# Optimization experiments

Hardware: AMD Instinct MI355X
Metric: run time of the kernel (lower is better)

The kernel has to match this reference:

```python
import jax, jax.numpy as jnp
import numpy as np

HEADS = 8
DIM_HEAD = 64
INNER = HEADS * DIM_HEAD  # 512
DIM = 256
MSA_H = 128  # number of MSA rows
MSA_W = 256  # sequence length


def setup_inputs() -> dict:
    key = jax.random.key(0)
    ks = jax.random.split(key, 8)
    n = MSA_H * MSA_W
    w_std = 0.02
    return {
        "x": jax.random.normal(ks[0], (1, n, DIM), dtype=jnp.float32),
        "wq_w": jax.random.normal(ks[1], (DIM, INNER), dtype=jnp.float32) * w_std,
        "wkv_w": jax.random.normal(ks[2], (DIM, 2 * INNER), dtype=jnp.float32) * w_std,
        "wout_w": jax.random.normal(ks[3], (INNER, DIM), dtype=jnp.float32) * w_std,
        "wout_b": jnp.zeros((DIM,), dtype=jnp.float32),
        "hq_w": jax.random.normal(ks[4], (DIM, INNER), dtype=jnp.float32) * w_std,
        "hkv_w": jax.random.normal(ks[5], (DIM, 2 * INNER), dtype=jnp.float32) * w_std,
        "hout_w": jax.random.normal(ks[6], (INNER, DIM), dtype=jnp.float32) * w_std,
        "hout_b": jnp.zeros((DIM,), dtype=jnp.float32),
        "msa_h": MSA_H,
        "msa_w": MSA_W,
    }


def reference(x, wq_w, wkv_w, wout_w, wout_b, hq_w, hkv_w, hout_w, hout_b, msa_h, msa_w):
    b, n, d = x.shape
    h, w = msa_h, msa_w
    scale = DIM_HEAD ** -0.5
    x4 = x.reshape(b, h, w, d)  # (b, rows, cols, dim)

    # ---- width attention: attend across MSA rows (h), independent per column (w) ----
    xw = jnp.swapaxes(x4, 1, 2)  # (b, w, h, d)
    q = (xw @ wq_w).reshape(b, w, h, HEADS, DIM_HEAD)
    kv = (xw @ wkv_w).reshape(b, w, h, 2, HEADS, DIM_HEAD)
    k, v = kv[..., 0, :, :], kv[..., 1, :, :]
    dots = jnp.einsum('bwiHd,bwjHd->bwHij', q, k) * scale  # (b, w, H, h, h)
    attn = jax.nn.softmax(dots, axis=-1)
    o = jnp.einsum('bwHij,bwjHd->bwiHd', attn, v).reshape(b, w, h, INNER)
    w_out = o @ wout_w + wout_b  # (b, w, h, d)
    w_out = jnp.swapaxes(w_out, 1, 2)  # (b, h, w, d)

    # ---- height attention: attend across columns (w), rows tied (tie_attn_dim = h) ----
    q = (x4 @ hq_w).reshape(b, h, w, HEADS, DIM_HEAD)
    kv = (x4 @ hkv_w).reshape(b, h, w, 2, HEADS, DIM_HEAD)
    k, v = kv[..., 0, :, :], kv[..., 1, :, :]
    tie_scale = scale * (h ** -0.5)
    # scores summed over tied row dim r: 'b r h i d, b r h j d -> b h i j'
    dots = jnp.einsum('briHd,brjHd->bHij', q, k) * tie_scale  # (b, H, w, w)
    attn = jax.nn.softmax(dots, axis=-1)
    o = jnp.einsum('bHij,brjHd->briHd', attn, v).reshape(b, h, w, INNER)
    h_out = o @ hout_w + hout_b  # (b, h, w, d)

    out = w_out + h_out
    return out.reshape(b, h * w, d)
```

## Files before the change

kernel.cpp:

```cpp
#include <hip/hip_runtime.h>

typedef short s16x8 __attribute__((ext_vector_type(8)));
typedef float f32x4 __attribute__((ext_vector_type(4)));

#define MFMA16(a, b, c) __builtin_amdgcn_mfma_f32_16x16x32_bf16((a), (b), (c), 0, 0, 0)

__device__ __forceinline__ unsigned short f2b(float f) {
  union { float f; unsigned int u; } v; v.f = f;
  unsigned int u = v.u;
  unsigned int r = (u + 0x7fffu + ((u >> 16) & 1u)) >> 16;
  return (unsigned short)r;
}
__device__ __forceinline__ float b2f(unsigned short b) {
  union { unsigned int u; float f; } v; v.u = ((unsigned int)b) << 16;
  return v.f;
}

__device__ __forceinline__ void gld_lds16(const void* g, void* l) {
  __builtin_amdgcn_global_load_lds(
      (const __attribute__((address_space(1))) unsigned int*)g,
      (__attribute__((address_space(3))) unsigned int*)l, 16, 0, 0);
}

__global__ __launch_bounds__(256) void cvt_x(const float* __restrict__ x,
                                             unsigned short* __restrict__ xb) {
  size_t i = ((size_t)blockIdx.x * 256 + threadIdx.x) * 4;
  float4 v = *(const float4*)(x + i);
  ushort4 o;
  o.x = f2b(v.x); o.y = f2b(v.y); o.z = f2b(v.z); o.w = f2b(v.w);
  *(ushort4*)(xb + i) = o;
}

__global__ __launch_bounds__(256) void build_wt(const float* __restrict__ wq,
                                                const float* __restrict__ wkv,
                                                const float* __restrict__ hq,
                                                const float* __restrict__ hkv,
                                                unsigned short* __restrict__ WT) {
  const int n = blockIdx.x, k = threadIdx.x;
  float v;
  if (n < 512)       v = wq [(size_t)k * 512  + n];
  else if (n < 1536) v = wkv[(size_t)k * 1024 + (n - 512)];
  else if (n < 2048) v = hq [(size_t)k * 512  + (n - 1536)];
  else               v = hkv[(size_t)k * 1024 + (n - 2048)];
  WT[(size_t)n * 256 + k] = f2b(v);
}

__global__ __launch_bounds__(256) void build_w2t(const float* __restrict__ wout,
                                                 const float* __restrict__ hout,
                                                 unsigned short* __restrict__ W2T) {
  const int n = blockIdx.x;
  for (int k = threadIdx.x; k < 1024; k += 256) {
    const float v = (k < 512) ? wout[(size_t)k * 256 + n] : hout[(size_t)(k - 512) * 256 + n];
    W2T[(size_t)n * 1024 + k] = f2b(v);
  }
}

__global__ __launch_bounds__(256) void gemm_qkv(const unsigned short* __restrict__ X,
                                                const unsigned short* __restrict__ WT,
                                                unsigned short* __restrict__ C,
                                                int branch) {
  __shared__ unsigned short As[128 * 32];
  __shared__ unsigned short Bs[128 * 32];
  const int tid = threadIdx.x, wave = tid >> 6, lane = tid & 63;
  const int q = lane >> 4, l = lane & 15;
  const int m0 = blockIdx.x * 128;
  const int n0 = blockIdx.y * 128;
  const int mt = (wave >> 1) * 64;
  const int nt = (wave & 1) * 64;
  const char* Xb = (const char*)X;
  const char* Wb = (const char*)WT;
  const int srow = wave * 32 + (lane >> 2);
  const int sboff = (lane & 3) * 16;
  char* AsB = (char*)As;
  char* BsB = (char*)Bs;
  f32x4 acc[4][4] = {};
#pragma unroll
  for (int ks = 0; ks < 8; ++ks) {
    const int kb = ks * 64;
    gld_lds16(Xb + (size_t)(m0 + srow) * 512 + kb + sboff, AsB + wave * 2048);
    gld_lds16(Xb + (size_t)(m0 + srow + 16) * 512 + kb + sboff, AsB + wave * 2048 + 1024);
    gld_lds16(Wb + (size_t)(n0 + srow) * 512 + kb + sboff, BsB + wave * 2048);
    gld_lds16(Wb + (size_t)(n0 + srow + 16) * 512 + kb + sboff, BsB + wave * 2048 + 1024);
    __syncthreads();
    s16x8 a[4], b[4];
#pragma unroll
    for (int i = 0; i < 4; ++i) a[i] = *(const s16x8*)(&As[(mt + i * 16 + l) * 32 + q * 8]);
#pragma unroll
    for (int j = 0; j < 4; ++j) b[j] = *(const s16x8*)(&Bs[(nt + j * 16 + l) * 32 + q * 8]);
#pragma unroll
    for (int i = 0; i < 4; ++i)
#pragma unroll
      for (int j = 0; j < 4; ++j) acc[i][j] = MFMA16(b[j], a[i], acc[i][j]);
    __syncthreads();
  }
#pragma unroll
  for (int i = 0; i < 4; ++i) {
    const int m = m0 + mt + i * 16 + l;
    const int mrow = (branch == 0) ? ((m & 255) * 8) : ((m >> 8) * 8);
    const int mcol = (branch == 0) ? (m >> 8) : (m & 255);
    const int mdim = (branch == 0) ? 128 : 256;
#pragma unroll
    for (int j = 0; j < 4; ++j) {
      const int n = n0 + nt + j * 16 + q * 4;
      const int part = n >> 9, H = (n & 511) >> 6, d = n & 63;
      ushort4 o;
      o.x = f2b(acc[i][j][0]); o.y = f2b(acc[i][j][1]);
      o.z = f2b(acc[i][j][2]); o.w = f2b(acc[i][j][3]);
      unsigned short* base = C + (size_t)part * 16777216;
      const size_t idx = ((size_t)(mrow + H) * mdim + mcol) * 64 + d;
      *(ushort4*)(base + idx) = o;
    }
  }
}

__global__ __launch_bounds__(256) void col_attn(const unsigned short* __restrict__ C,
                                                unsigned short* __restrict__ O) {
  __shared__ unsigned short Sp[128 * 136];
  __shared__ unsigned short Vt[64 * 136];
  const int w = blockIdx.x, H = blockIdx.y;
  const int tid = threadIdx.x, wave = tid >> 6, lane = tid & 63;
  const int q = lane >> 4, l = lane & 15;
  const size_t slab = (size_t)(w * 8 + H) * 8192;
  const unsigned short* Qs = C + slab;
  const unsigned short* Ks = C + 16777216 + slab;
  const unsigned short* Vs = C + 33554432 + slab;
  for (int u = tid; u < 1024; u += 256) {
    const int j = u >> 3, db = u & 7;
    s16x8 v = *(const s16x8*)(Vs + j * 64 + db * 8);
#pragma unroll
    for (int t = 0; t < 8; ++t) Vt[(db * 8 + t) * 136 + j] = v[t];
  }
  const int m0 = wave * 32;
  f32x4 acc[2][8] = {};
#pragma unroll
  for (int ks = 0; ks < 2; ++ks) {
    const int kk = ks * 32 + q * 8;
    s16x8 a[2], b[8];
#pragma unroll
    for (int i = 0; i < 2; ++i) a[i] = *(const s16x8*)(Qs + (m0 + i * 16 + l) * 64 + kk);
#pragma unroll
    for (int j = 0; j < 8; ++j) b[j] = *(const s16x8*)(Ks + (j * 16 + l) * 64 + kk);
#pragma unroll
    for (int i = 0; i < 2; ++i)
#pragma unroll
      for (int j = 0; j < 8; ++j) acc[i][j] = MFMA16(a[i], b[j], acc[i][j]);
  }
#pragma unroll
  for (int i = 0; i < 2; ++i)
#pragma unroll
    for (int r = 0; r < 4; ++r) {
      float v[8];
#pragma unroll
      for (int j = 0; j < 8; ++j) v[j] = acc[i][j][r] * 0.125f;
      float mx = fmaxf(fmaxf(fmaxf(v[0], v[1]), fmaxf(v[2], v[3])),
                       fmaxf(fmaxf(v[4], v[5]), fmaxf(v[6], v[7])));
      mx = fmaxf(mx, __shfl_xor(mx, 1));
      mx = fmaxf(mx, __shfl_xor(mx, 2));
      mx = fmaxf(mx, __shfl_xor(mx, 4));
      mx = fmaxf(mx, __shfl_xor(mx, 8));
      float s = 0.f;
#pragma unroll
      for (int j = 0; j < 8; ++j) { v[j] = __expf(v[j] - mx); s += v[j]; }
      s += __shfl_xor(s, 1);
      s += __shfl_xor(s, 2);
      s += __shfl_xor(s, 4);
      s += __shfl_xor(s, 8);
      const float inv = 1.0f / s;
      const int row = m0 + i * 16 + q * 4 + r;
#pragma unroll
      for (int j = 0; j < 8; ++j) Sp[row * 136 + j * 16 + l] = f2b(v[j] * inv);
    }
  __syncthreads();
  f32x4 o[2][4] = {};
#pragma unroll
  for (int ks = 0; ks < 4; ++ks) {
    const int kk = ks * 32 + q * 8;
    s16x8 a[2], b[4];
#pragma unroll
    for (int i = 0; i < 2; ++i) a[i] = *(const s16x8*)(&Sp[(m0 + i * 16 + l) * 136 + kk]);
#pragma unroll
    for (int j = 0; j < 4; ++j) b[j] = *(const s16x8*)(&Vt[(j * 16 + l) * 136 + kk]);
#pragma unroll
    for (int i = 0; i < 2; ++i)
#pragma unroll
      for (int j = 0; j < 4; ++j) o[i][j] = MFMA16(a[i], b[j], o[i][j]);
  }
#pragma unroll
  for (int i = 0; i < 2; ++i)
#pragma unroll
    for (int j = 0; j < 4; ++j)
#pragma unroll
      for (int r = 0; r < 4; ++r) {
        const int row = m0 + i * 16 + q * 4 + r;
        const int d = j * 16 + l;
        O[(size_t)(row * 256 + w) * 1024 + H * 64 + d] = f2b(o[i][j][r]);
      }
}

__global__ __launch_bounds__(256) void row_dots(const unsigned short* __restrict__ C,
                                                float* __restrict__ dp) {
  const int H = blockIdx.z;
  const int r0 = blockIdx.y * 16;
  const int ti = blockIdx.x & 1, tj = blockIdx.x >> 1;
  const int tid = threadIdx.x, wave = tid >> 6, lane = tid & 63;
  const int q = lane >> 4, l = lane & 15;
  const int m0 = ti * 128 + (wave >> 1) * 64;
  const int n0 = tj * 128 + (wave & 1) * 64;
  const unsigned short* Qh = C;
  const unsigned short* Kh = C + 16777216;
  f32x4 acc[4][4] = {};
  for (int ks = 0; ks < 32; ++ks) {
    const int k = ks * 32 + q * 8;
    const int rr = r0 + (k >> 6), d = k & 63;
    const size_t slab = (size_t)(rr * 8 + H) * 16384;
    s16x8 a[4], b[4];
#pragma unroll
    for (int i = 0; i < 4; ++i) a[i] = *(const s16x8*)(Qh + slab + (m0 + i * 16 + l) * 64 + d);
#pragma unroll
    for (int j = 0; j < 4; ++j) b[j] = *(const s16x8*)(Kh + slab + (n0 + j * 16 + l) * 64 + d);
#pragma unroll
    for (int i = 0; i < 4; ++i)
#pragma unroll
      for (int j = 0; j < 4; ++j) acc[i][j] = MFMA16(a[i], b[j], acc[i][j]);
  }
  float* outp = dp + ((size_t)blockIdx.y * 8 + H) * 65536;
#pragma unroll
  for (int i = 0; i < 4; ++i)
#pragma unroll
    for (int j = 0; j < 4; ++j)
#pragma unroll
      for (int r = 0; r < 4; ++r)
        outp[(size_t)(m0 + i * 16 + q * 4 + r) * 256 + n0 + j * 16 + l] = acc[i][j][r];
}

__global__ __launch_bounds__(256) void row_softmax(const float* __restrict__ dp,
                                                   unsigned short* __restrict__ attn) {
  const int row = blockIdx.x;
  const int H = row >> 8, i = row & 255;
  const int t = threadIdx.x, wave = t >> 6, lane = t & 63;
  __shared__ float red[8];
  float v = 0.f;
#pragma unroll
  for (int c = 0; c < 8; ++c) v += dp[((size_t)c * 8 + H) * 65536 + (size_t)i * 256 + t];
  v *= 1.1048543456e-2f;
  float m = v;
  for (int o = 32; o > 0; o >>= 1) m = fmaxf(m, __shfl_xor(m, o, 64));
  if (lane == 0) red[wave] = m;
  __syncthreads();
  const float M = fmaxf(fmaxf(red[0], red[1]), fmaxf(red[2], red[3]));
  const float e = __expf(v - M);
  float s = e;
  for (int o = 32; o > 0; o >>= 1) s += __shfl_xor(s, o, 64);
  if (lane == 0) red[4 + wave] = s;
  __syncthreads();
  const float S = red[4] + red[5] + red[6] + red[7];
  attn[(size_t)row * 256 + t] = f2b(e / S);
}

__global__ __launch_bounds__(256) void row_pv(const unsigned short* __restrict__ C,
                                              const unsigned short* __restrict__ attn,
                                              unsigned short* __restrict__ O) {
  __shared__ unsigned short Vt[64 * 264];
  const int r = blockIdx.x, H = blockIdx.y;
  const int tid = threadIdx.x, wave = tid >> 6, lane = tid & 63;
  const int q = lane >> 4, l = lane & 15;
  const unsigned short* Vs = C + 33554432 + (size_t)(r * 8 + H) * 16384;
  for (int u = tid; u < 2048; u += 256) {
    const int j = u >> 3, db = u & 7;
    s16x8 v = *(const s16x8*)(Vs + j * 64 + db * 8);
#pragma unroll
    for (int t = 0; t < 8; ++t) Vt[(db * 8 + t) * 264 + j] = v[t];
  }
  __syncthreads();
  const unsigned short* A = attn + (size_t)H * 65536;
  const int m0 = wave * 64;
  f32x4 acc[4][4] = {};
#pragma unroll
  for (int ks = 0; ks < 8; ++ks) {
    const int kk = ks * 32 + q * 8;
    s16x8 a[4], b[4];
#pragma unroll
    for (int i = 0; i < 4; ++i) a[i] = *(const s16x8*)(A + (size_t)(m0 + i * 16 + l) * 256 + kk);
#pragma unroll
    for (int j = 0; j < 4; ++j) b[j] = *(const s16x8*)(&Vt[(j * 16 + l) * 264 + kk]);
#pragma unroll
    for (int i = 0; i < 4; ++i)
#pragma unroll
      for (int j = 0; j < 4; ++j) acc[i][j] = MFMA16(a[i], b[j], acc[i][j]);
  }
#pragma unroll
  for (int i = 0; i < 4; ++i)
#pragma unroll
    for (int j = 0; j < 4; ++j)
#pragma unroll
      for (int rr = 0; rr < 4; ++rr) {
        const int iw = m0 + i * 16 + q * 4 + rr;
        const int d = j * 16 + l;
        O[(size_t)(r * 256 + iw) * 1024 + 512 + H * 64 + d] = f2b(acc[i][j][rr]);
      }
}

__global__ __launch_bounds__(256) void out_proj(const unsigned short* __restrict__ O,
                                                const unsigned short* __restrict__ W2T,
                                                const float* __restrict__ bw,
                                                const float* __restrict__ bh,
                                                float* __restrict__ out) {
  __shared__ unsigned short As[128 * 32];
  __shared__ unsigned short Bs[128 * 32];
  const int tid = threadIdx.x, wave = tid >> 6, lane = tid & 63;
  const int q = lane >> 4, l = lane & 15;
  const int m0 = blockIdx.x * 128;
  const int n0 = blockIdx.y * 128;
  const int mt = (wave >> 1) * 64;
  const int nt = (wave & 1) * 64;
  const char* Ob = (const char*)O;
  const char* Wb = (const char*)W2T;
  const int srow = wave * 32 + (lane >> 2);
  const int sboff = (lane & 3) * 16;
  char* AsB = (char*)As;
  char* BsB = (char*)Bs;
  f32x4 acc[4][4] = {};
  for (int ks = 0; ks < 32; ++ks) {
    const int kb = ks * 64;
    gld_lds16(Ob + (size_t)(m0 + srow) * 2048 + kb + sboff, AsB + wave * 2048);
    gld_lds16(Ob + (size_t)(m0 + srow + 16) * 2048 + kb + sboff, AsB + wave * 2048 + 1024);
    gld_lds16(Wb + (size_t)(n0 + srow) * 2048 + kb + sboff, BsB + wave * 2048);
    gld_lds16(Wb + (size_t)(n0 + srow + 16) * 2048 + kb + sboff, BsB + wave * 2048 + 1024);
    __syncthreads();
    s16x8 a[4], b[4];
#pragma unroll
    for (int i = 0; i < 4; ++i) a[i] = *(const s16x8*)(&As[(mt + i * 16 + l) * 32 + q * 8]);
#pragma unroll
    for (int j = 0; j < 4; ++j) b[j] = *(const s16x8*)(&Bs[(nt + j * 16 + l) * 32 + q * 8]);
#pragma unroll
    for (int i = 0; i < 4; ++i)
#pragma unroll
      for (int j = 0; j < 4; ++j) acc[i][j] = MFMA16(b[j], a[i], acc[i][j]);
    __syncthreads();
  }
#pragma unroll
  for (int i = 0; i < 4; ++i) {
    const int m = m0 + mt + i * 16 + l;
#pragma unroll
    for (int j = 0; j < 4; ++j) {
      const int col = n0 + nt + j * 16 + q * 4;
      const float4 bwv = *(const float4*)(bw + col);
      const float4 bhv = *(const float4*)(bh + col);
      float4 ov;
      ov.x = acc[i][j][0] + bwv.x + bhv.x;
      ov.y = acc[i][j][1] + bwv.y + bhv.y;
      ov.z = acc[i][j][2] + bwv.z + bhv.z;
      ov.w = acc[i][j][3] + bwv.w + bhv.w;
      *(float4*)(out + (size_t)m * 256 + col) = ov;
    }
  }
}

extern "C" void kernel_launch(void* const* d_in, const int* in_sizes, int n_in,
                              void* d_out, int out_size, void* d_ws, size_t ws_size,
                              hipStream_t stream) {
  const float* x    = (const float*)d_in[0];
  const float* wq   = (const float*)d_in[1];
  const float* wkv  = (const float*)d_in[2];
  const float* wout = (const float*)d_in[3];
  const float* bw   = (const float*)d_in[4];
  const float* hq   = (const float*)d_in[5];
  const float* hkv  = (const float*)d_in[6];
  const float* hout = (const float*)d_in[7];
  const float* bh   = (const float*)d_in[8];
  float* out = (float*)d_out;

  char* ws = (char*)d_ws;
  unsigned short* x_bf  = (unsigned short*)(ws);
  unsigned short* WcatT = (unsigned short*)(ws + 16777216);
  unsigned short* W2T   = (unsigned short*)(ws + 18350080);
  float*          dp    = (float*)(ws + 18874368);
  unsigned short* attn  = (unsigned short*)(ws + 35651584);
  unsigned short* Ocat  = (unsigned short*)(ws + 36700160);
  unsigned short* Cproj = (unsigned short*)(ws + 103809024);

  cvt_x<<<8192, 256, 0, stream>>>(x, x_bf);
  build_wt<<<3072, 256, 0, stream>>>(wq, wkv, hq, hkv, WcatT);
  build_w2t<<<256, 256, 0, stream>>>(wout, hout, W2T);

  gemm_qkv<<<dim3(256, 12), 256, 0, stream>>>(x_bf, WcatT, Cproj, 0);
  col_attn<<<dim3(256, 8), 256, 0, stream>>>(Cproj, Ocat);
  gemm_qkv<<<dim3(256, 12), 256, 0, stream>>>(x_bf, WcatT + 1536 * 256, Cproj, 1);
  row_dots<<<dim3(4, 8, 8), 256, 0, stream>>>(Cproj, dp);
  row_softmax<<<2048, 256, 0, stream>>>(dp, attn);
  row_pv<<<dim3(128, 8), 256, 0, stream>>>(Cproj, attn, Ocat);
  out_proj<<<dim3(256, 2), 256, 0, stream>>>(Ocat, W2T, bw, bh, out);
}
```

Before: 355.4 us.

## Replace LDS-staged GEMM tiles with direct global-to-register fragment loads

Both the QKV projection GEMM and the output projection GEMM stop staging A/B tiles through shared memory with global_load_lds and barriers. Each wave now loads its MFMA fragments straight from global memory. The block tile becomes 64 rows by 256 columns split across four waves, and the grid is reshaped to match. This removes the per-k-step barriers and LDS traffic. In exchange, the X rows are fetched redundantly by every wave, and the loads are 16-byte strided row reads that depend on L1/L2 hits for reuse.

```diff
diff --git a/kernel.cpp b/kernel.cpp
--- a/kernel.cpp
+++ b/kernel.cpp
@@ -14,12 +14,6 @@
 __device__ __forceinline__ float b2f(unsigned short b) {
   union { unsigned int u; float f; } v; v.u = ((unsigned int)b) << 16;
   return v.f;
-}
-
-__device__ __forceinline__ void gld_lds16(const void* g, void* l) {
-  __builtin_amdgcn_global_load_lds(
-      (const __attribute__((address_space(1))) unsigned int*)g,
-      (__attribute__((address_space(3))) unsigned int*)l, 16, 0, 0);
 }
 
 __global__ __launch_bounds__(256) void cvt_x(const float* __restrict__ x,
@@ -59,49 +53,35 @@
                                                 const unsigned short* __restrict__ WT,
                                                 unsigned short* __restrict__ C,
                                                 int branch) {
-  __shared__ unsigned short As[128 * 32];
-  __shared__ unsigned short Bs[128 * 32];
-  const int tid = threadIdx.x, wave = tid >> 6, lane = tid & 63;
-  const int q = lane >> 4, l = lane & 15;
-  const int m0 = blockIdx.x * 128;
-  const int n0 = blockIdx.y * 128;
-  const int mt = (wave >> 1) * 64;
-  const int nt = (wave & 1) * 64;
-  const char* Xb = (const char*)X;
-  const char* Wb = (const char*)WT;
-  const int srow = wave * 32 + (lane >> 2);
-  const int sboff = (lane & 3) * 16;
-  char* AsB = (char*)As;
-  char* BsB = (char*)Bs;
+  const int tid = threadIdx.x, wave = tid >> 6, lane = tid & 63;
+  const int q = lane >> 4, l = lane & 15;
+  const int m0 = blockIdx.x * 64;
+  const int nw = blockIdx.y * 256 + wave * 64;
   f32x4 acc[4][4] = {};
 #pragma unroll
   for (int ks = 0; ks < 8; ++ks) {
-    const int kb = ks * 64;
-    gld_lds16(Xb + (size_t)(m0 + srow) * 512 + kb + sboff, AsB + wave * 2048);
-    gld_lds16(Xb + (size_t)(m0 + srow + 16) * 512 + kb + sboff, AsB + wave * 2048 + 1024);
-    gld_lds16(Wb + (size_t)(n0 + srow) * 512 + kb + sboff, BsB + wave * 2048);
-    gld_lds16(Wb + (size_t)(n0 + srow + 16) * 512 + kb + sboff, BsB + wave * 2048 + 1024);
-    __syncthreads();
+    const int kk = ks * 32 + q * 8;
     s16x8 a[4], b[4];
 #pragma unroll
-    for (int i = 0; i < 4; ++i) a[i] = *(const s16x8*)(&As[(mt + i * 16 + l) * 32 + q * 8]);
-#pragma unroll
-    for (int j = 0; j < 4; ++j) b[j] = *(const s16x8*)(&Bs[(nt + j * 16 + l) * 32 + q * 8]);
+    for (int i = 0; i < 4; ++i)
+      a[i] = *(const s16x8*)(X + (size_t)(m0 + i * 16 + l) * 256 + kk);
+#pragma unroll
+    for (int j = 0; j < 4; ++j)
+      b[j] = *(const s16x8*)(WT + (size_t)(nw + j * 16 + l) * 256 + kk);
 #pragma unroll
     for (int i = 0; i < 4; ++i)
 #pragma unroll
       for (int j = 0; j < 4; ++j) acc[i][j] = MFMA16(b[j], a[i], acc[i][j]);
-    __syncthreads();
   }
 #pragma unroll
   for (int i = 0; i < 4; ++i) {
-    const int m = m0 + mt + i * 16 + l;
+    const int m = m0 + i * 16 + l;
     const int mrow = (branch == 0) ? ((m & 255) * 8) : ((m >> 8) * 8);
     const int mcol = (branch == 0) ? (m >> 8) : (m & 255);
     const int mdim = (branch == 0) ? 128 : 256;
 #pragma unroll
     for (int j = 0; j < 4; ++j) {
-      const int n = n0 + nt + j * 16 + q * 4;
+      const int n = nw + j * 16 + q * 4;
       const int part = n >> 9, H = (n & 511) >> 6, d = n & 63;
       ushort4 o;
       o.x = f2b(acc[i][j][0]); o.y = f2b(acc[i][j][1]);
@@ -305,45 +285,32 @@
                                                 const float* __restrict__ bw,
                                                 const float* __restrict__ bh,
                                                 float* __restrict__ out) {
-  __shared__ unsigned short As[128 * 32];
-  __shared__ unsigned short Bs[128 * 32];
-  const int tid = threadIdx.x, wave = tid >> 6, lane = tid & 63;
-  const int q = lane >> 4, l = lane & 15;
-  const int m0 = blockIdx.x * 128;
-  const int n0 = blockIdx.y * 128;
-  const int mt = (wave >> 1) * 64;
-  const int nt = (wave & 1) * 64;
-  const char* Ob = (const char*)O;
-  const char* Wb = (const char*)W2T;
-  const int srow = wave * 32 + (lane >> 2);
-  const int sboff = (lane & 3) * 16;
-  char* AsB = (char*)As;
-  char* BsB = (char*)Bs;
+  const int tid = threadIdx.x, wave = tid >> 6, lane = tid & 63;
+  const int q = lane >> 4, l = lane & 15;
+  const int m0 = blockIdx.x * 64;
+  const int nw = wave * 64;
   f32x4 acc[4][4] = {};
+#pragma unroll
   for (int ks = 0; ks < 32; ++ks) {
-    const int kb = ks * 64;
-    gld_lds16(Ob + (size_t)(m0 + srow) * 2048 + kb + sboff, AsB + wave * 2048);
-    gld_lds16(Ob + (size_t)(m0 + srow + 16) * 2048 + kb + sboff, AsB + wave * 2048 + 1024);
-    gld_lds16(Wb + (size_t)(n0 + srow) * 2048 + kb + sboff, BsB + wave * 2048);
-    gld_lds16(Wb + (size_t)(n0 + srow + 16) * 2048 + kb + sboff, BsB + wave * 2048 + 1024);
-    __syncthreads();
+    const int kk = ks * 32 + q * 8;
     s16x8 a[4], b[4];
 #pragma unroll
-    for (int i = 0; i < 4; ++i) a[i] = *(const s16x8*)(&As[(mt + i * 16 + l) * 32 + q * 8]);
-#pragma unroll
-    for (int j = 0; j < 4; ++j) b[j] = *(const s16x8*)(&Bs[(nt + j * 16 + l) * 32 + q * 8]);
+    for (int i = 0; i < 4; ++i)
+      a[i] = *(const s16x8*)(O + (size_t)(m0 + i * 16 + l) * 1024 + kk);
+#pragma unroll
+    for (int j = 0; j < 4; ++j)
+      b[j] = *(const s16x8*)(W2T + (size_t)(nw + j * 16 + l) * 1024 + kk);
 #pragma unroll
     for (int i = 0; i < 4; ++i)
 #pragma unroll
       for (int j = 0; j < 4; ++j) acc[i][j] = MFMA16(b[j], a[i], acc[i][j]);
-    __syncthreads();
   }
 #pragma unroll
   for (int i = 0; i < 4; ++i) {
-    const int m = m0 + mt + i * 16 + l;
+    const int m = m0 + i * 16 + l;
 #pragma unroll
     for (int j = 0; j < 4; ++j) {
-      const int col = n0 + nt + j * 16 + q * 4;
+      const int col = nw + j * 16 + q * 4;
       const float4 bwv = *(const float4*)(bw + col);
       const float4 bhv = *(const float4*)(bh + col);
       float4 ov;
@@ -383,11 +350,11 @@
   build_wt<<<3072, 256, 0, stream>>>(wq, wkv, hq, hkv, WcatT);
   build_w2t<<<256, 256, 0, stream>>>(wout, hout, W2T);
 
-  gemm_qkv<<<dim3(256, 12), 256, 0, stream>>>(x_bf, WcatT, Cproj, 0);
+  gemm_qkv<<<dim3(512, 6), 256, 0, stream>>>(x_bf, WcatT, Cproj, 0);
   col_attn<<<dim3(256, 8), 256, 0, stream>>>(Cproj, Ocat);
-  gemm_qkv<<<dim3(256, 12), 256, 0, stream>>>(x_bf, WcatT + 1536 * 256, Cproj, 1);
+  gemm_qkv<<<dim3(512, 6), 256, 0, stream>>>(x_bf, WcatT + 1536 * 256, Cproj, 1);
   row_dots<<<dim3(4, 8, 8), 256, 0, stream>>>(Cproj, dp);
   row_softmax<<<2048, 256, 0, stream>>>(dp, attn);
   row_pv<<<dim3(128, 8), 256, 0, stream>>>(Cproj, attn, Ocat);
-  out_proj<<<dim3(256, 2), 256, 0, stream>>>(Ocat, W2T, bw, bh, out);
-}
+  out_proj<<<512, 256, 0, stream>>>(Ocat, W2T, bw, bh, out);
+}
```

New measurement: 496.1 us. 1.4x slower.

## Fuse column-branch QKV projection with column attention in one kernel

Applied to the files above, without the earlier changes.

Replaces the separate QKV GEMM and column-attention kernels with one kernel per column. It loads the 128x256 x slice into LDS, computes Q/K/V per head with MFMA, and runs the softmax and PV product entirely in LDS. This removes the global round-trip of the column-branch Q/K/V (about 100MB of bf16 writes and reads) and one launch. In exchange there are only 256 blocks using ~150KB of LDS each, so occupancy is one block per CU. Weights are read from global/L2 per head, with a serial head loop and syncthreads between stages.

```diff
diff --git a/kernel.cpp b/kernel.cpp
--- a/kernel.cpp
+++ b/kernel.cpp
@@ -52,6 +52,126 @@
   for (int k = threadIdx.x; k < 1024; k += 256) {
     const float v = (k < 512) ? wout[(size_t)k * 256 + n] : hout[(size_t)(k - 512) * 256 + n];
     W2T[(size_t)n * 1024 + k] = f2b(v);
+  }
+}
+
+__global__ __launch_bounds__(512) void fused_col(const unsigned short* __restrict__ X,
+                                                 const unsigned short* __restrict__ WT,
+                                                 unsigned short* __restrict__ O) {
+  __shared__ __align__(16) char lds[154624];
+  unsigned short* Sp = (unsigned short*)(lds + 119808);
+  const int w = blockIdx.x;
+  const int tid = threadIdx.x, wave = tid >> 6, lane = tid & 63;
+  const int q = lane >> 4, l = lane & 15;
+  const int mt = wave * 16;
+  const char* Xl = lds;
+  char* Ql = lds + 65536;
+  char* Kl = lds + 83968;
+  char* Vt = lds + 102400;
+  {
+    const char* Xb = (const char*)X;
+#pragma unroll
+    for (int it = 0; it < 8; ++it) {
+      const int u = it * 512 + wave * 64 + lane;
+      const int row = u >> 5, c = u & 31;
+      gld_lds16(Xb + ((size_t)(row * 256 + w)) * 512 + ((c ^ (row & 7)) * 16),
+                (char*)lds + (it * 512 + wave * 64) * 16);
+    }
+  }
+  __syncthreads();
+  for (int H = 0; H < 8; ++H) {
+    f32x4 accq[4] = {}, acck[4] = {}, accv[4] = {};
+#pragma unroll
+    for (int ks = 0; ks < 8; ++ks) {
+      const int kk = ks * 32 + q * 8;
+      const int c = kk >> 3;
+      const int row = mt + l;
+      s16x8 a = *(const s16x8*)(Xl + (size_t)row * 512 + ((c ^ (row & 7)) * 16));
+      s16x8 bq[4], bk[4], bv[4];
+#pragma unroll
+      for (int j = 0; j < 4; ++j) {
+        bq[j] = *(const s16x8*)(WT + (size_t)(H * 64 + j * 16 + l) * 256 + kk);
+        bk[j] = *(const s16x8*)(WT + (size_t)(512 + H * 64 + j * 16 + l) * 256 + kk);
+        bv[j] = *(const s16x8*)(WT + (size_t)(1024 + H * 64 + j * 16 + l) * 256 + kk);
+      }
+#pragma unroll
+      for (int j = 0; j < 4; ++j) {
+        accq[j] = MFMA16(bq[j], a, accq[j]);
+        acck[j] = MFMA16(bk[j], a, acck[j]);
+        accv[j] = MFMA16(a, bv[j], accv[j]);
+      }
+    }
+#pragma unroll
+    for (int j = 0; j < 4; ++j) {
+      ushort4 oq, ok, ov;
+      oq.x = f2b(accq[j][0]); oq.y = f2b(accq[j][1]); oq.z = f2b(accq[j][2]); oq.w = f2b(accq[j][3]);
+      ok.x = f2b(acck[j][0]); ok.y = f2b(acck[j][1]); ok.z = f2b(acck[j][2]); ok.w = f2b(acck[j][3]);
+      ov.x = f2b(accv[j][0]); ov.y = f2b(accv[j][1]); ov.z = f2b(accv[j][2]); ov.w = f2b(accv[j][3]);
+      *(ushort4*)(Ql + (size_t)(mt + l) * 144 + (j * 16 + q * 4) * 2) = oq;
+      *(ushort4*)(Kl + (size_t)(mt + l) * 144 + (j * 16 + q * 4) * 2) = ok;
+      *(ushort4*)(Vt + (size_t)(j * 16 + l) * 272 + (mt + q * 4) * 2) = ov;
+    }
+    __syncthreads();
+    {
+      f32x4 s[8] = {};
+#pragma unroll
+      for (int ks = 0; ks < 2; ++ks) {
+        const int kb = ks * 64 + q * 16;
+        s16x8 aq = *(const s16x8*)(Ql + (size_t)(mt + l) * 144 + kb);
+        s16x8 bk[8];
+#pragma unroll
+        for (int j = 0; j < 8; ++j)
+          bk[j] = *(const s16x8*)(Kl + (size_t)(j * 16 + l) * 144 + kb);
+#pragma unroll
+        for (int j = 0; j < 8; ++j) s[j] = MFMA16(aq, bk[j], s[j]);
+      }
+#pragma unroll
+      for (int r = 0; r < 4; ++r) {
+        float v[8];
+#pragma unroll
+        for (int j = 0; j < 8; ++j) v[j] = s[j][r] * 0.125f;
+        float mx = fmaxf(fmaxf(fmaxf(v[0], v[1]), fmaxf(v[2], v[3])),
+                         fmaxf(fmaxf(v[4], v[5]), fmaxf(v[6], v[7])));
+        mx = fmaxf(mx, __shfl_xor(mx, 1));
+        mx = fmaxf(mx, __shfl_xor(mx, 2));
+        mx = fmaxf(mx, __shfl_xor(mx, 4));
+        mx = fmaxf(mx, __shfl_xor(mx, 8));
+        float sm = 0.f;
+#pragma unroll
+        for (int j = 0; j < 8; ++j) { v[j] = __expf(v[j] - mx); sm += v[j]; }
+        sm += __shfl_xor(sm, 1);
+        sm += __shfl_xor(sm, 2);
+        sm += __shfl_xor(sm, 4);
+        sm += __shfl_xor(sm, 8);
+        const float inv = 1.0f / sm;
+        const int row = mt + q * 4 + r;
+#pragma unroll
+        for (int j = 0; j < 8; ++j) Sp[row * 136 + j * 16 + l] = f2b(v[j] * inv);
+      }
+    }
+    __syncthreads();
+    {
+      f32x4 o[4] = {};
+#pragma unroll
+      for (int ks = 0; ks < 4; ++ks) {
+        const int kb = ks * 64 + q * 16;
+        s16x8 ap = *(const s16x8*)((const char*)Sp + (size_t)(mt + l) * 272 + kb);
+        s16x8 bv[4];
+#pragma unroll
+        for (int j = 0; j < 4; ++j)
+          bv[j] = *(const s16x8*)(Vt + (size_t)(j * 16 + l) * 272 + kb);
+#pragma unroll
+        for (int j = 0; j < 4; ++j) o[j] = MFMA16(ap, bv[j], o[j]);
+      }
+#pragma unroll
+      for (int j = 0; j < 4; ++j)
+#pragma unroll
+        for (int r = 0; r < 4; ++r) {
+          const int row = mt + q * 4 + r;
+          O[(size_t)(row * 256 + w) * 1024 + H * 64 + j * 16 + l] = f2b(o[j][r]);
+        }
+    }
+    __syncthreads();
   }
 }
 
@@ -111,90 +231,6 @@
       *(ushort4*)(base + idx) = o;
     }
   }
-}
-
-__global__ __launch_bounds__(256) void col_attn(const unsigned short* __restrict__ C,
-                                                unsigned short* __restrict__ O) {
-  __shared__ unsigned short Sp[128 * 136];
-  __shared__ unsigned short Vt[64 * 136];
-  const int w = blockIdx.x, H = blockIdx.y;
-  const int tid = threadIdx.x, wave = tid >> 6, lane = tid & 63;
-  const int q = lane >> 4, l = lane & 15;
-  const size_t slab = (size_t)(w * 8 + H) * 8192;
-  const unsigned short* Qs = C + slab;
-  const unsigned short* Ks = C + 16777216 + slab;
-  const unsigned short* Vs = C + 33554432 + slab;
-  for (int u = tid; u < 1024; u += 256) {
-    const int j = u >> 3, db = u & 7;
-    s16x8 v = *(const s16x8*)(Vs + j * 64 + db * 8);
-#pragma unroll
-    for (int t = 0; t < 8; ++t) Vt[(db * 8 + t) * 136 + j] = v[t];
-  }
-  const int m0 = wave * 32;
-  f32x4 acc[2][8] = {};
-#pragma unroll
-  for (int ks = 0; ks < 2; ++ks) {
-    const int kk = ks * 32 + q * 8;
-    s16x8 a[2], b[8];
-#pragma unroll
-    for (int i = 0; i < 2; ++i) a[i] = *(const s16x8*)(Qs + (m0 + i * 16 + l) * 64 + kk);
-#pragma unroll
-    for (int j = 0; j < 8; ++j) b[j] = *(const s16x8*)(Ks + (j * 16 + l) * 64 + kk);
-#pragma unroll
-    for (int i = 0; i < 2; ++i)
-#pragma unroll
-      for (int j = 0; j < 8; ++j) acc[i][j] = MFMA16(a[i], b[j], acc[i][j]);
-  }
-#pragma unroll
-  for (int i = 0; i < 2; ++i)
-#pragma unroll
-    for (int r = 0; r < 4; ++r) {
-      float v[8];
-#pragma unroll
-      for (int j = 0; j < 8; ++j) v[j] = acc[i][j][r] * 0.125f;
-      float mx = fmaxf(fmaxf(fmaxf(v[0], v[1]), fmaxf(v[2], v[3])),
-                       fmaxf(fmaxf(v[4], v[5]), fmaxf(v[6], v[7])));
-      mx = fmaxf(mx, __shfl_xor(mx, 1));
-      mx = fmaxf(mx, __shfl_xor(mx, 2));
-      mx = fmaxf(mx, __shfl_xor(mx, 4));
-      mx = fmaxf(mx, __shfl_xor(mx, 8));
-      float s = 0.f;
-#pragma unroll
-      for (int j = 0; j < 8; ++j) { v[j] = __expf(v[j] - mx); s += v[j]; }
-      s += __shfl_xor(s, 1);
-      s += __shfl_xor(s, 2);
-      s += __shfl_xor(s, 4);
-      s += __shfl_xor(s, 8);
-      const float inv = 1.0f / s;
-      const int row = m0 + i * 16 + q * 4 + r;
-#pragma unroll
-      for (int j = 0; j < 8; ++j) Sp[row * 136 + j * 16 + l] = f2b(v[j] * inv);
-    }
-  __syncthreads();
-  f32x4 o[2][4] = {};
-#pragma unroll
-  for (int ks = 0; ks < 4; ++ks) {
-    const int kk = ks * 32 + q * 8;
-    s16x8 a[2], b[4];
-#pragma unroll
-    for (int i = 0; i < 2; ++i) a[i] = *(const s16x8*)(&Sp[(m0 + i * 16 + l) * 136 + kk]);
-#pragma unroll
-    for (int j = 0; j < 4; ++j) b[j] = *(const s16x8*)(&Vt[(j * 16 + l) * 136 + kk]);
-#pragma unroll
-    for (int i = 0; i < 2; ++i)
-#pragma unroll
-      for (int j = 0; j < 4; ++j) o[i][j] = MFMA16(a[i], b[j], o[i][j]);
-  }
-#pragma unroll
-  for (int i = 0; i < 2; ++i)
-#pragma unroll
-    for (int j = 0; j < 4; ++j)
-#pragma unroll
-      for (int r = 0; r < 4; ++r) {
-        const int row = m0 + i * 16 + q * 4 + r;
-        const int d = j * 16 + l;
-        O[(size_t)(row * 256 + w) * 1024 + H * 64 + d] = f2b(o[i][j][r]);
-      }
 }
 
 __global__ __launch_bounds__(256) void row_dots(const unsigned short* __restrict__ C,
@@ -383,8 +419,7 @@
   build_wt<<<3072, 256, 0, stream>>>(wq, wkv, hq, hkv, WcatT);
   build_w2t<<<256, 256, 0, stream>>>(wout, hout, W2T);
 
-  gemm_qkv<<<dim3(256, 12), 256, 0, stream>>>(x_bf, WcatT, Cproj, 0);
-  col_attn<<<dim3(256, 8), 256, 0, stream>>>(Cproj, Ocat);
+  fused_col<<<256, 512, 0, stream>>>(x_bf, WcatT, Ocat);
   gemm_qkv<<<dim3(256, 12), 256, 0, stream>>>(x_bf, WcatT + 1536 * 256, Cproj, 1);
   row_dots<<<dim3(4, 8, 8), 256, 0, stream>>>(Cproj, dp);
   row_softmax<<<2048, 256, 0, stream>>>(dp, attn);
```

New measurement: 466.9 us. 31.4% more time.

## Load full-K GEMM tiles into XOR-swizzled LDS once and reorder grid

Applied to the files above, without the earlier changes.

The QKV projection GEMM now loads the whole K=256 extent of both 128-row A and B tiles into LDS in one pass, with an XOR swizzle on 16-byte chunks to avoid bank conflicts. This removes the per-k-step barrier pairs. The grid is transposed so consecutive blocks share the same X row tile across N tiles, which should improve L2 reuse of X. LDS use rises to 128 KB per block, so each CU holds at most one block and there is no overlap between loads and MFMA within a block.

```diff
diff --git a/kernel.cpp b/kernel.cpp
--- a/kernel.cpp
+++ b/kernel.cpp
@@ -59,39 +59,45 @@
                                                 const unsigned short* __restrict__ WT,
                                                 unsigned short* __restrict__ C,
                                                 int branch) {
-  __shared__ unsigned short As[128 * 32];
-  __shared__ unsigned short Bs[128 * 32];
-  const int tid = threadIdx.x, wave = tid >> 6, lane = tid & 63;
-  const int q = lane >> 4, l = lane & 15;
-  const int m0 = blockIdx.x * 128;
-  const int n0 = blockIdx.y * 128;
+  __shared__ __align__(16) unsigned short As[128 * 256];
+  __shared__ __align__(16) unsigned short Bs[128 * 256];
+  const int tid = threadIdx.x, wave = tid >> 6, lane = tid & 63;
+  const int q = lane >> 4, l = lane & 15;
+  const int n0 = blockIdx.x * 128;
+  const int m0 = blockIdx.y * 128;
   const int mt = (wave >> 1) * 64;
   const int nt = (wave & 1) * 64;
   const char* Xb = (const char*)X;
   const char* Wb = (const char*)WT;
-  const int srow = wave * 32 + (lane >> 2);
-  const int sboff = (lane & 3) * 16;
   char* AsB = (char*)As;
   char* BsB = (char*)Bs;
+#pragma unroll
+  for (int it = 0; it < 16; ++it) {
+    const int u = it * 256 + wave * 64 + lane;
+    const int row = u >> 5, c = u & 31;
+    const size_t goff = (size_t)row * 512 + ((c ^ (row & 7)) * 16);
+    gld_lds16(Xb + (size_t)m0 * 512 + goff, AsB + it * 4096 + wave * 1024);
+    gld_lds16(Wb + (size_t)n0 * 512 + goff, BsB + it * 4096 + wave * 1024);
+  }
+  __syncthreads();
   f32x4 acc[4][4] = {};
 #pragma unroll
   for (int ks = 0; ks < 8; ++ks) {
-    const int kb = ks * 64;
-    gld_lds16(Xb + (size_t)(m0 + srow) * 512 + kb + sboff, AsB + wave * 2048);
-    gld_lds16(Xb + (size_t)(m0 + srow + 16) * 512 + kb + sboff, AsB + wave * 2048 + 1024);
-    gld_lds16(Wb + (size_t)(n0 + srow) * 512 + kb + sboff, BsB + wave * 2048);
-    gld_lds16(Wb + (size_t)(n0 + srow + 16) * 512 + kb + sboff, BsB + wave * 2048 + 1024);
-    __syncthreads();
     s16x8 a[4], b[4];
 #pragma unroll
-    for (int i = 0; i < 4; ++i) a[i] = *(const s16x8*)(&As[(mt + i * 16 + l) * 32 + q * 8]);
-#pragma unroll
-    for (int j = 0; j < 4; ++j) b[j] = *(const s16x8*)(&Bs[(nt + j * 16 + l) * 32 + q * 8]);
+    for (int i = 0; i < 4; ++i) {
+      const int row = mt + i * 16 + l;
+      a[i] = *(const s16x8*)(AsB + (size_t)row * 512 + (((ks * 4 + q) ^ (row & 7)) * 16));
+    }
+#pragma unroll
+    for (int j = 0; j < 4; ++j) {
+      const int row = nt + j * 16 + l;
+      b[j] = *(const s16x8*)(BsB + (size_t)row * 512 + (((ks * 4 + q) ^ (row & 7)) * 16));
+    }
 #pragma unroll
     for (int i = 0; i < 4; ++i)
 #pragma unroll
       for (int j = 0; j < 4; ++j) acc[i][j] = MFMA16(b[j], a[i], acc[i][j]);
-    __syncthreads();
   }
 #pragma unroll
   for (int i = 0; i < 4; ++i) {
@@ -383,9 +389,9 @@
   build_wt<<<3072, 256, 0, stream>>>(wq, wkv, hq, hkv, WcatT);
   build_w2t<<<256, 256, 0, stream>>>(wout, hout, W2T);
 
-  gemm_qkv<<<dim3(256, 12), 256, 0, stream>>>(x_bf, WcatT, Cproj, 0);
+  gemm_qkv<<<dim3(12, 256), 256, 0, stream>>>(x_bf, WcatT, Cproj, 0);
   col_attn<<<dim3(256, 8), 256, 0, stream>>>(Cproj, Ocat);
-  gemm_qkv<<<dim3(256, 12), 256, 0, stream>>>(x_bf, WcatT + 1536 * 256, Cproj, 1);
+  gemm_qkv<<<dim3(12, 256), 256, 0, stream>>>(x_bf, WcatT + 1536 * 256, Cproj, 1);
   row_dots<<<dim3(4, 8, 8), 256, 0, stream>>>(Cproj, dp);
   row_softmax<<<2048, 256, 0, stream>>>(dp, attn);
   row_pv<<<dim3(128, 8), 256, 0, stream>>>(Cproj, attn, Ocat);
```

Measured after the change: 388.8 us. +9.4%, slower.
